# Kernel tuning notes

Hardware: AMD Instinct MI355X
Metric: run time of the kernel (lower is better)

Reference implementation:

```python
import jax, jax.numpy as jnp
import numpy as np

NB_LAYERS, KSIZE = 4, 5
DILATIONS = [1, 2, 4, 8]
NEG_SLOPE = 0.1
BN_EPS = 1e-5


def _cont_conv(times, feats, mask, dilation, p):
    """One ContConv1d layer: causal gather of time-diffs -> kernel MLP -> weighted aggregate + skip + BN."""
    k1W, k1b, k2W, k2b, k3W, k3b, skipW, skipb, gamma, beta = p
    bs, L, Cin = feats.shape
    Cout = skipW.shape[1]
    lags = jnp.arange(KSIZE) * dilation                    # (K,) include_zero_lag=True -> lag 0 included
    idx = jnp.arange(L)[None, :] - lags[:, None]           # (K, L) causal neighbor indices
    valid = idx >= 0
    idx_c = jnp.clip(idx, 0, L - 1)
    g_times = times[:, idx_c]                              # (bs, K, L)
    g_feats = feats[:, idx_c, :]                           # (bs, K, L, Cin)
    g_mask = (mask[:, idx_c] & valid[None] & mask[:, None, :]).astype(feats.dtype)
    dt = (times[:, None, :] - g_times) * g_mask            # (bs, K, L) zeroed where invalid
    # kernel MLP: scalar time-diff -> (Cin, Cout) mixing matrix
    h = jax.nn.leaky_relu(dt[..., None] @ k1W + k1b, NEG_SLOPE)
    h = jax.nn.leaky_relu(h @ k2W + k2b, NEG_SLOPE)
    kv = (h @ k3W + k3b).reshape(bs, KSIZE, L, Cin, Cout) * g_mask[..., None, None]
    out = jnp.einsum('bklc,bklcd->bld', g_feats, kv)       # aggregate over taps and input channels
    out = out + feats @ skipW + skipb                      # 1x1-conv skip connection
    mu = out.mean((0, 1))                                  # BatchNorm1d (training-mode batch stats)
    var = out.var((0, 1))
    return (out - mu) * jax.lax.rsqrt(var + BN_EPS) * gamma + beta


def _ccnn_forward(event_times, event_types, emb, k1W, k1b, k2W, k2b, k3W, k3b, skipW, skipb, gamma, beta):
    bs = event_times.shape[0]
    emb = emb.at[0].set(0.0)                               # padding_idx = 0
    times = jnp.concatenate([jnp.zeros((bs, 1), event_times.dtype), event_times], axis=1)
    bos = jnp.full((bs, 1), jnp.max(event_types) + 1, dtype=event_types.dtype)
    types = jnp.concatenate([bos, event_types], axis=1)
    mask = times != 0                                      # BOS (t=0) masked, as in the original
    enc = emb[types]                                       # (bs, L+1, C)
    for i in range(NB_LAYERS):
        p = (k1W[i], k1b[i], k2W[i], k2b[i], k3W[i], k3b[i], skipW[i], skipb[i], gamma[i], beta[i])
        enc = jax.nn.leaky_relu(_cont_conv(times, enc, mask, DILATIONS[i], p), NEG_SLOPE)
    return enc


def setup_inputs() -> dict:
    key = jax.random.key(0)
    ks = jax.random.split(key, 12)
    bs, L, C, H, num_types = 8, 2048, 32, 16, 100
    s = 0.05
    gaps = jax.random.uniform(ks[0], (bs, L)) * 0.1 + 0.01
    times = jnp.cumsum(gaps, axis=1)                       # strictly increasing positive event times
    types = jax.random.randint(ks[1], (bs, L), 0, num_types) + 1   # 1..num_types
    pad = jnp.arange(L) >= int(0.9 * L)
    times = jnp.where(pad[None, :], 0.0, times).astype(jnp.float32)
    types = jnp.where(pad[None, :], 0, types).astype(jnp.int32)
    return {
        'event_times': times,
        'event_types': types,
        'emb': jax.random.normal(ks[2], (num_types + 2, C)) * s,
        'k1W': jax.random.normal(ks[3], (NB_LAYERS, 1, H)) * s,
        'k1b': jnp.zeros((NB_LAYERS, H)),
        'k2W': jax.random.normal(ks[4], (NB_LAYERS, H, H)) * s,
        'k2b': jnp.zeros((NB_LAYERS, H)),
        'k3W': jax.random.normal(ks[5], (NB_LAYERS, H, C * C)) * s,
        'k3b': jnp.zeros((NB_LAYERS, C * C)),
        'skipW': jax.random.normal(ks[6], (NB_LAYERS, C, C)) * s,
        'skipb': jnp.zeros((NB_LAYERS, C)),
        'gamma': jnp.ones((NB_LAYERS, C)),
        'beta': jnp.zeros((NB_LAYERS, C)),
    }


def reference(event_times, event_types, emb, k1W, k1b, k2W, k2b, k3W, k3b, skipW, skipb, gamma, beta):
    return _ccnn_forward(event_times, event_types, emb, k1W, k1b, k2W, k2b, k3W, k3b, skipW, skipb, gamma, beta)
```

## Files before the change

kernel.cpp:

```cpp
#include <hip/hip_runtime.h>
#include <stdint.h>

#define NB_LAYERS 4
#define KSIZE 5
#define BSZ 8
#define LIN 2048
#define LSEQ 2049
#define CCH 32
#define HCH 16
#define MROWS (BSZ*LSEQ)
#define NTILES ((MROWS+15)/16)
#define NEG 0.1f
#define BNEPS 1e-5f
#define CONVGRID 129
#define CONVBLK 512
#define NFRAG 36
#define WT_HALVES (NFRAG*64*8)

typedef _Float16 h2v __attribute__((ext_vector_type(2)));
typedef _Float16 h8v __attribute__((ext_vector_type(8)));
typedef float    f4v __attribute__((ext_vector_type(4)));

union H8 { h8v v; h2v h[4]; };

static __device__ __forceinline__ h2v mkh2(float a, float b) {
  h2v r; r[0] = (_Float16)a; r[1] = (_Float16)b; return r;
}

static __device__ __forceinline__ void wt_decode(
    int g, const float* __restrict__ k3Wl, const float* __restrict__ k3bl,
    const float* __restrict__ skipWl, int& halfidx, float& val) {
  int n, k;
  if (g < 16384)      { n = g & 31; int c = (g >> 5) & 31; int h = g >> 10; k = h * 32 + c; val = k3Wl[g]; }
  else if (g < 17408) { int g2 = g - 16384; n = g2 & 31; int c = g2 >> 5; k = 512 + c; val = k3bl[g2]; }
  else                { int g2 = g - 17408; n = g2 & 31; int c = g2 >> 5; k = 544 + c; val = skipWl[g2]; }
  int m = n & 15, a = n >> 4, qq = (k >> 3) & 3, hh = k & 7;
  int f = (k < 512) ? ((k >> 5) * 2 + a) : ((k < 544) ? (32 + a) : (34 + a));
  halfidx = f * 512 + ((qq << 4) | m) * 8 + hh;
}

template<int MODE>
__global__ __launch_bounds__(CONVBLK) void conv_kernel(
    const float* __restrict__ enc_in,
    const int*   __restrict__ types,
    const float* __restrict__ emb,
    float* __restrict__ enc_out,
    const float* __restrict__ etimes,
    const float* __restrict__ k1Wp, const float* __restrict__ k1bp,
    const float* __restrict__ k2Wp, const float* __restrict__ k2bp,
    const float* __restrict__ k3W, const float* __restrict__ k3b,
    const float* __restrict__ skipW,
    _Float16* __restrict__ Wt,
    const float* __restrict__ stats_prev,
    const float* __restrict__ partials_prev,
    float* __restrict__ stats_out,
    float* __restrict__ partials_out,
    float* __restrict__ stats_zero,
    const float* __restrict__ gamma_prev, const float* __restrict__ beta_prev,
    int dil)
{
  __shared__ h8v swh[(CONVBLK/64) * KSIZE * 16 * 2];
  __shared__ alignas(16) float sW[304];
  __shared__ float sst[64];
  __shared__ float sbn[64];

  const int tid  = threadIdx.x;
  const int lane = tid & 63;
  const int wv   = tid >> 6;
  const int m    = lane & 15;
  const int q    = lane >> 4;

  if (tid < 64) { sst[tid] = 0.f; sbn[tid] = 0.f; }
  if (tid < 16) { sW[tid] = k1Wp[tid]; sW[16 + tid] = k1bp[tid]; sW[32 + tid] = k2bp[tid]; }
  if (tid >= 64 && tid < 320) sW[48 + tid - 64] = k2Wp[tid - 64];

  if (MODE == 0) {
    if (blockIdx.x == 0 && tid < 192) stats_zero[tid] = 0.f;
    int id2 = blockIdx.x * CONVBLK + tid;
    if (id2 < 3 * WT_HALVES) {
      int layer = 1 + id2 / WT_HALVES;
      int g = id2 - (layer - 1) * WT_HALVES;
      int hi; float val;
      wt_decode(g, k3W + layer * 16384, k3b + layer * 1024, skipW + layer * 1024, hi, val);
      Wt[(layer - 1) * WT_HALVES + hi] = (_Float16)val;
    }
  }
  __syncthreads();

  if (MODE == 1 && partials_prev) {
    float v = 0.f;
#pragma unroll 4
    for (int i = tid; i < CONVGRID * 64; i += CONVBLK) v += partials_prev[i];
    atomicAdd(&sbn[tid & 63], v);
    __syncthreads();
  }

  float sc8[8], ob8[8];
  if (MODE == 1) {
    const float inv = 1.f / (float)MROWS;
#pragma unroll
    for (int j = 0; j < 8; j++) {
      int c = q * 8 + j;
      float s1 = partials_prev ? sbn[c]      : stats_prev[c];
      float s2 = partials_prev ? sbn[32 + c] : stats_prev[32 + c];
      float mu = s1 * inv;
      float var = s2 * inv - mu * mu;
      float sc = gamma_prev[c] * rsqrtf(var + BNEPS);
      sc8[j] = sc; ob8[j] = beta_prev[c] - mu * sc;
    }
  }

  const int tile = blockIdx.x * (CONVBLK / 64) + wv;
  const bool deadtile = (tile >= NTILES);

  if (!deadtile) {
    int row = tile * 16 + m;
    bool rvalid = row < MROWS;
    int rowc = min(row, MROWS - 1);
    int b = rowc / LSEQ, pos = rowc % LSEQ;
    float t_l = (pos == 0) ? 0.f : etimes[b * LIN + pos - 1];
    bool mask_l = rvalid && (t_l != 0.f);

    int bosv = 0;
    if (MODE == 0) {
      if (__ballot(pos == 0)) {
        const int4* tp = (const int4*)types;
        int mx = 0;
#pragma unroll 4
        for (int i = lane; i < (BSZ * LIN) / 4; i += 64) {
          int4 v = tp[i];
          mx = max(mx, max(max(v.x, v.y), max(v.z, v.w)));
        }
#pragma unroll
        for (int off = 32; off; off >>= 1) mx = max(mx, __shfl_xor(mx, off, 64));
        bosv = mx + 1;
      }
    }

    int jcs[KSIZE]; float tjv[KSIZE];
#pragma unroll
    for (int tap = 0; tap < KSIZE; tap++) {
      int j = pos - tap * dil;
      int jc = max(j, 0); jcs[tap] = jc;
      tjv[tap] = (jc == 0) ? 0.f : etimes[b * LIN + jc - 1];
    }
    float4 fa[KSIZE], fbv[KSIZE];
    int tts[KSIZE];
    if (MODE == 0) {
#pragma unroll
      for (int tap = 0; tap < KSIZE; tap++) {
        int jc = jcs[tap];
        tts[tap] = (jc > 0) ? types[b * LIN + jc - 1] : ((tap == 0) ? bosv : 0);
      }
#pragma unroll
      for (int tap = 0; tap < KSIZE; tap++) {
        const float* ep = emb + tts[tap] * CCH + q * 8;
        fa[tap] = *(const float4*)ep; fbv[tap] = *(const float4*)(ep + 4);
      }
    } else {
#pragma unroll
      for (int tap = 0; tap < KSIZE; tap++) {
        const float* fp = enc_in + (b * LSEQ + jcs[tap]) * CCH + q * 8;
        fa[tap] = *(const float4*)fp; fbv[tap] = *(const float4*)(fp + 4);
      }
    }

    h2v fh[KSIZE][4];
    h2v fself[4];
    float Fb[8];
#pragma unroll
    for (int jj = 0; jj < 8; jj++) Fb[jj] = 0.f;

#pragma unroll
    for (int tap = 0; tap < KSIZE; tap++) {
      bool gm = mask_l && (pos - tap * dil >= 0) && (tjv[tap] != 0.f);
      float fv[8] = {fa[tap].x, fa[tap].y, fa[tap].z, fa[tap].w,
                     fbv[tap].x, fbv[tap].y, fbv[tap].z, fbv[tap].w};
      if (MODE == 0) {
        float zf = (tts[tap] != 0) ? 1.f : 0.f;
#pragma unroll
        for (int jj = 0; jj < 8; jj++) fv[jj] *= zf;
      } else {
#pragma unroll
        for (int jj = 0; jj < 8; jj++) {
          float x = fmaf(fv[jj], sc8[jj], ob8[jj]);
          fv[jj] = fmaxf(x, NEG * x);
        }
      }
      if (tap == 0) {
        float rv = rvalid ? 1.f : 0.f;
#pragma unroll
        for (int p2 = 0; p2 < 4; p2++) fself[p2] = mkh2(fv[2*p2] * rv, fv[2*p2+1] * rv);
      }
      float g = gm ? 1.f : 0.f;
#pragma unroll
      for (int jj = 0; jj < 8; jj++) Fb[jj] += g * fv[jj];
#pragma unroll
      for (int p2 = 0; p2 < 4; p2++) fh[tap][p2] = mkh2(fv[2*p2], fv[2*p2+1]);
    }

#pragma unroll
    for (int rep = 0; rep < 2; rep++) {
      const int jt = rep ? (KSIZE - 1) : (lane >> 4);
      const bool act = rep ? (lane < 16) : true;
      int j2 = pos - jt * dil;
      int jc2 = max(j2, 0);
      float tj2 = (jc2 == 0) ? 0.f : etimes[b * LIN + jc2 - 1];
      bool g2 = act && mask_l && (j2 >= 0) && (tj2 != 0.f);
      float dt = g2 ? (t_l - tj2) : 0.f;

      H8 w0, w1;
      if (__ballot(g2)) {
        const f4v* k1wv = (const f4v*)&sW[0];
        const f4v* k1bv = (const f4v*)&sW[16];
        const f4v* k2bv = (const f4v*)&sW[32];
        float h1[HCH], h2[HCH];
#pragma unroll
        for (int h4 = 0; h4 < 4; h4++) {
          f4v cw = k1wv[h4], cb = k1bv[h4], c2 = k2bv[h4];
#pragma unroll
          for (int r = 0; r < 4; r++) {
            float x = fmaf(dt, cw[r], cb[r]);
            h1[h4*4+r] = fmaxf(x, NEG * x);
            h2[h4*4+r] = c2[r];
          }
        }
#pragma unroll
        for (int hp = 0; hp < HCH; hp++) {
          float hv = h1[hp];
          const f4v* kk = (const f4v*)&sW[48 + hp * 16];
#pragma unroll
          for (int h4 = 0; h4 < 4; h4++) {
            f4v c = kk[h4];
#pragma unroll
            for (int r = 0; r < 4; r++) h2[h4*4+r] = fmaf(hv, c[r], h2[h4*4+r]);
          }
        }
        float g = g2 ? 1.f : 0.f;
#pragma unroll
        for (int p2 = 0; p2 < 4; p2++) {
          float a0 = h2[2*p2];     a0 = fmaxf(a0, NEG * a0) * g;
          float a1 = h2[2*p2+1];   a1 = fmaxf(a1, NEG * a1) * g;
          w0.h[p2] = mkh2(a0, a1);
          float b0 = h2[8+2*p2];   b0 = fmaxf(b0, NEG * b0) * g;
          float b1 = h2[8+2*p2+1]; b1 = fmaxf(b1, NEG * b1) * g;
          w1.h[p2] = mkh2(b0, b1);
        }
      } else {
#pragma unroll
        for (int p2 = 0; p2 < 4; p2++) { w0.h[p2] = mkh2(0.f, 0.f); w1.h[p2] = mkh2(0.f, 0.f); }
      }
      if (act) {
        int base = ((wv * KSIZE + jt) * 16 + m) * 2;
        swh[base] = w0.v; swh[base + 1] = w1.v;
      }
    }
    __syncthreads();

    h2v wh[KSIZE][8];
#pragma unroll
    for (int tap = 0; tap < KSIZE; tap++) {
      int base = ((wv * KSIZE + tap) * 16 + m) * 2;
      H8 a0, a1; a0.v = swh[base]; a1.v = swh[base + 1];
#pragma unroll
      for (int p2 = 0; p2 < 4; p2++) { wh[tap][p2] = a0.h[p2]; wh[tap][4+p2] = a1.h[p2]; }
    }

    f4v aP = {0,0,0,0}, aQ = {0,0,0,0}, bP = {0,0,0,0}, bQ = {0,0,0,0};

#pragma unroll
    for (int ks = 0; ks < 16; ks++) {
      H8 bf0, bf1, af;
      if (MODE == 0) {
        const float* wp = k3W + ks * 1024 + (q * 8) * 32 + m;
#pragma unroll
        for (int p2 = 0; p2 < 4; p2++) {
          bf0.h[p2] = mkh2(wp[(2*p2) * 32],      wp[(2*p2+1) * 32]);
          bf1.h[p2] = mkh2(wp[(2*p2) * 32 + 16], wp[(2*p2+1) * 32 + 16]);
        }
      } else {
        bf0.v = *(const h8v*)(Wt + (size_t)((2*ks + 0) * 64 + lane) * 8);
        bf1.v = *(const h8v*)(Wt + (size_t)((2*ks + 1) * 64 + lane) * 8);
      }
      h2v u0 = mkh2(0.f,0.f), u1 = mkh2(0.f,0.f), u2 = mkh2(0.f,0.f), u3 = mkh2(0.f,0.f);
#pragma unroll
      for (int tap = 0; tap < KSIZE; tap++) {
        _Float16 w = wh[tap][ks >> 1][ks & 1];
        h2v wd; wd[0] = w; wd[1] = w;
        u0 += wd * fh[tap][0];
        u1 += wd * fh[tap][1];
        u2 += wd * fh[tap][2];
        u3 += wd * fh[tap][3];
      }
      af.h[0] = u0; af.h[1] = u1; af.h[2] = u2; af.h[3] = u3;
      if (ks & 1) {
        aQ = __builtin_amdgcn_mfma_f32_16x16x32_f16(af.v, bf0.v, aQ, 0, 0, 0);
        bQ = __builtin_amdgcn_mfma_f32_16x16x32_f16(af.v, bf1.v, bQ, 0, 0, 0);
      } else {
        aP = __builtin_amdgcn_mfma_f32_16x16x32_f16(af.v, bf0.v, aP, 0, 0, 0);
        bP = __builtin_amdgcn_mfma_f32_16x16x32_f16(af.v, bf1.v, bP, 0, 0, 0);
      }
    }
    {
      H8 bf0, bf1, af;
      if (MODE == 0) {
        const float* kp = k3b + (q * 8) * 32 + m;
#pragma unroll
        for (int p2 = 0; p2 < 4; p2++) {
          bf0.h[p2] = mkh2(kp[(2*p2) * 32],      kp[(2*p2+1) * 32]);
          bf1.h[p2] = mkh2(kp[(2*p2) * 32 + 16], kp[(2*p2+1) * 32 + 16]);
        }
      } else {
        bf0.v = *(const h8v*)(Wt + (size_t)(32 * 64 + lane) * 8);
        bf1.v = *(const h8v*)(Wt + (size_t)(33 * 64 + lane) * 8);
      }
#pragma unroll
      for (int p2 = 0; p2 < 4; p2++) af.h[p2] = mkh2(Fb[2*p2], Fb[2*p2+1]);
      aP = __builtin_amdgcn_mfma_f32_16x16x32_f16(af.v, bf0.v, aP, 0, 0, 0);
      bP = __builtin_amdgcn_mfma_f32_16x16x32_f16(af.v, bf1.v, bP, 0, 0, 0);
    }
    {
      H8 bf0, bf1, af;
      if (MODE == 0) {
        const float* sp = skipW + (q * 8) * 32 + m;
#pragma unroll
        for (int p2 = 0; p2 < 4; p2++) {
          bf0.h[p2] = mkh2(sp[(2*p2) * 32],      sp[(2*p2+1) * 32]);
          bf1.h[p2] = mkh2(sp[(2*p2) * 32 + 16], sp[(2*p2+1) * 32 + 16]);
        }
      } else {
        bf0.v = *(const h8v*)(Wt + (size_t)(34 * 64 + lane) * 8);
        bf1.v = *(const h8v*)(Wt + (size_t)(35 * 64 + lane) * 8);
      }
      af.h[0] = fself[0]; af.h[1] = fself[1]; af.h[2] = fself[2]; af.h[3] = fself[3];
      aQ = __builtin_amdgcn_mfma_f32_16x16x32_f16(af.v, bf0.v, aQ, 0, 0, 0);
      bQ = __builtin_amdgcn_mfma_f32_16x16x32_f16(af.v, bf1.v, bQ, 0, 0, 0);
    }
    f4v acc0 = aP + aQ;
    f4v acc1 = bP + bQ;

    float s0 = 0.f, s1 = 0.f, s2 = 0.f, s3 = 0.f;
#pragma unroll
    for (int r = 0; r < 4; r++) {
      float v0 = acc0[r], v1 = acc1[r];
      s0 += v0; s1 += v0 * v0; s2 += v1; s3 += v1 * v1;
      int rd = tile * 16 + q * 4 + r;
      if (rd < MROWS) {
        enc_out[rd * CCH + m] = v0;
        enc_out[rd * CCH + 16 + m] = v1;
      }
    }
    s0 += __shfl_xor(s0, 16, 64); s0 += __shfl_xor(s0, 32, 64);
    s1 += __shfl_xor(s1, 16, 64); s1 += __shfl_xor(s1, 32, 64);
    s2 += __shfl_xor(s2, 16, 64); s2 += __shfl_xor(s2, 32, 64);
    s3 += __shfl_xor(s3, 16, 64); s3 += __shfl_xor(s3, 32, 64);
    if (q == 0) {
      atomicAdd(&sst[m], s0);
      atomicAdd(&sst[32 + m], s1);
      atomicAdd(&sst[16 + m], s2);
      atomicAdd(&sst[48 + m], s3);
    }
  } else {
    __syncthreads();
  }
  __syncthreads();
  if (tid < 64) {
    if (MODE == 0) partials_out[blockIdx.x * 64 + tid] = sst[tid];
    else           atomicAdd(&stats_out[tid], sst[tid]);
  }
}

__global__ __launch_bounds__(256) void bn_kernel(
    const float* __restrict__ x, float* __restrict__ out,
    const float* __restrict__ stats,
    const float* __restrict__ gamma, const float* __restrict__ beta) {
  int idx0 = blockIdx.x * 256 + threadIdx.x;
  int c0 = (idx0 * 4) & 31;
  const float inv = 1.f / (float)MROWS;
  float sc[4], ob[4];
#pragma unroll
  for (int r = 0; r < 4; r++) {
    int c = c0 + r;
    float mu = stats[c] * inv;
    float var = stats[32 + c] * inv - mu * mu;
    sc[r] = gamma[c] * rsqrtf(var + BNEPS);
    ob[r] = beta[c] - mu * sc[r];
  }
  for (int i = idx0; i < (MROWS * CCH) / 4; i += 256 * 256) {
    float4 v = ((const float4*)x)[i];
    float4 o;
    o.x = fmaf(v.x, sc[0], ob[0]); o.x = fmaxf(o.x, NEG * o.x);
    o.y = fmaf(v.y, sc[1], ob[1]); o.y = fmaxf(o.y, NEG * o.y);
    o.z = fmaf(v.z, sc[2], ob[2]); o.z = fmaxf(o.z, NEG * o.z);
    o.w = fmaf(v.w, sc[3], ob[3]); o.w = fmaxf(o.w, NEG * o.w);
    ((float4*)out)[i] = o;
  }
}

extern "C" void kernel_launch(void* const* d_in, const int* in_sizes, int n_in,
                              void* d_out, int out_size, void* d_ws, size_t ws_size,
                              hipStream_t stream) {
  (void)in_sizes; (void)n_in; (void)out_size; (void)ws_size;
  const float* event_times = (const float*)d_in[0];
  const int*   event_types = (const int*)d_in[1];
  const float* emb   = (const float*)d_in[2];
  const float* k1W   = (const float*)d_in[3];
  const float* k1b   = (const float*)d_in[4];
  const float* k2W   = (const float*)d_in[5];
  const float* k2b   = (const float*)d_in[6];
  const float* k3W   = (const float*)d_in[7];
  const float* k3b   = (const float*)d_in[8];
  const float* skipW = (const float*)d_in[9];
  const float* gamma = (const float*)d_in[11];
  const float* beta  = (const float*)d_in[12];

  float* enc_a = (float*)d_ws;
  float* enc_b = enc_a + (size_t)MROWS * CCH;
  float* stats = enc_b + (size_t)MROWS * CCH;
  float* partials0 = stats + NB_LAYERS * 64;
  _Float16* Wt = (_Float16*)(((uintptr_t)(partials0 + CONVGRID * 64) + 255) & ~(uintptr_t)255);

  conv_kernel<0><<<CONVGRID, CONVBLK, 0, stream>>>(
      nullptr, event_types, emb, enc_b, event_times,
      k1W, k1b, k2W, k2b, k3W, k3b, skipW, Wt,
      nullptr, nullptr, nullptr, partials0, stats + 64,
      nullptr, nullptr, 1);

  conv_kernel<1><<<CONVGRID, CONVBLK, 0, stream>>>(
      enc_b, nullptr, nullptr, enc_a, event_times,
      k1W + HCH, k1b + HCH, k2W + HCH*HCH, k2b + HCH,
      nullptr, nullptr, nullptr, Wt + 0 * WT_HALVES,
      nullptr, partials0, stats + 64, nullptr, nullptr,
      gamma + 0 * CCH, beta + 0 * CCH, 2);

  conv_kernel<1><<<CONVGRID, CONVBLK, 0, stream>>>(
      enc_a, nullptr, nullptr, enc_b, event_times,
      k1W + 2*HCH, k1b + 2*HCH, k2W + 2*HCH*HCH, k2b + 2*HCH,
      nullptr, nullptr, nullptr, Wt + 1 * WT_HALVES,
      stats + 64, nullptr, stats + 128, nullptr, nullptr,
      gamma + 1 * CCH, beta + 1 * CCH, 4);

  conv_kernel<1><<<CONVGRID, CONVBLK, 0, stream>>>(
      enc_b, nullptr, nullptr, enc_a, event_times,
      k1W + 3*HCH, k1b + 3*HCH, k2W + 3*HCH*HCH, k2b + 3*HCH,
      nullptr, nullptr, nullptr, Wt + 2 * WT_HALVES,
      stats + 128, nullptr, stats + 192, nullptr, nullptr,
      gamma + 2 * CCH, beta + 2 * CCH, 8);

  bn_kernel<<<256, 256, 0, stream>>>(enc_a, (float*)d_out,
      stats + 192, gamma + 3 * CCH, beta + 3 * CCH);
}
```

Before: 149.9 us.

## Stage fp16 weight fragments in LDS and rebalance kernel-MLP jobs across block

In MODE 1 the block now copies the pre-packed fp16 weight fragments (about 36 KB) from global memory into shared memory once, and the MFMA B-operands read from LDS instead of global. The per-tap kernel MLP work (5 taps x 16 rows per wave) is now spread across all threads of the block as 640 jobs, not done per wave with a mostly idle second pass, and the sync is restructured to match. The aim is to cut redundant global weight reads and improve lane utilization. The cost is a large LDS allocation that may reduce occupancy, plus extra index arithmetic and a second etimes gather per job.

```diff
diff --git a/kernel.cpp b/kernel.cpp
--- a/kernel.cpp
+++ b/kernel.cpp
@@ -14,6 +14,8 @@
 #define BNEPS 1e-5f
 #define CONVGRID 129
 #define CONVBLK 512
+#define NWAVES (CONVBLK/64)
+#define NJOBS (NWAVES*KSIZE*16)
 #define NFRAG 36
 #define WT_HALVES (NFRAG*64*8)
 
@@ -50,7 +52,7 @@
     const float* __restrict__ k2Wp, const float* __restrict__ k2bp,
     const float* __restrict__ k3W, const float* __restrict__ k3b,
     const float* __restrict__ skipW,
-    _Float16* __restrict__ Wt,
+    _Float16* __restrict__ WtG,
     const float* __restrict__ stats_prev,
     const float* __restrict__ partials_prev,
     float* __restrict__ stats_out,
@@ -59,7 +61,8 @@
     const float* __restrict__ gamma_prev, const float* __restrict__ beta_prev,
     int dil)
 {
-  __shared__ h8v swh[(CONVBLK/64) * KSIZE * 16 * 2];
+  __shared__ h8v Wl[(MODE == 1) ? (NFRAG * 64) : 1];
+  __shared__ h8v swh[NWAVES * KSIZE * 16 * 2];
   __shared__ alignas(16) float sW[304];
   __shared__ float sst[64];
   __shared__ float sbn[64];
@@ -69,20 +72,29 @@
   const int wv   = tid >> 6;
   const int m    = lane & 15;
   const int q    = lane >> 4;
+  const int bid  = blockIdx.x;
 
   if (tid < 64) { sst[tid] = 0.f; sbn[tid] = 0.f; }
   if (tid < 16) { sW[tid] = k1Wp[tid]; sW[16 + tid] = k1bp[tid]; sW[32 + tid] = k2bp[tid]; }
   if (tid >= 64 && tid < 320) sW[48 + tid - 64] = k2Wp[tid - 64];
 
   if (MODE == 0) {
-    if (blockIdx.x == 0 && tid < 192) stats_zero[tid] = 0.f;
-    int id2 = blockIdx.x * CONVBLK + tid;
+    if (bid == 0 && tid < 192) stats_zero[tid] = 0.f;
+    int id2 = bid * CONVBLK + tid;
     if (id2 < 3 * WT_HALVES) {
       int layer = 1 + id2 / WT_HALVES;
       int g = id2 - (layer - 1) * WT_HALVES;
       int hi; float val;
       wt_decode(g, k3W + layer * 16384, k3b + layer * 1024, skipW + layer * 1024, hi, val);
-      Wt[(layer - 1) * WT_HALVES + hi] = (_Float16)val;
+      WtG[(layer - 1) * WT_HALVES + hi] = (_Float16)val;
+    }
+  } else {
+    const float4* src = (const float4*)WtG;
+    float4* dst = (float4*)Wl;
+#pragma unroll
+    for (int i = 0; i < 5; i++) {
+      int idx = tid + i * CONVBLK;
+      if (idx < WT_HALVES / 8) dst[idx] = src[idx];
     }
   }
   __syncthreads();
@@ -110,17 +122,20 @@
     }
   }
 
-  const int tile = blockIdx.x * (CONVBLK / 64) + wv;
+  const int tile = bid * NWAVES + wv;
   const bool deadtile = (tile >= NTILES);
 
+  int row = tile * 16 + m;
+  bool rvalid = row < MROWS;
+  int rowc = min(row, MROWS - 1);
+  int b = rowc / LSEQ, pos = rowc % LSEQ;
+  float t_l = (pos == 0) ? 0.f : etimes[b * LIN + pos - 1];
+  bool mask_l = rvalid && (t_l != 0.f);
+
+  float4 fa[KSIZE], fbv[KSIZE];
+  int tts[KSIZE];
+  int jcs[KSIZE]; float tjv[KSIZE];
   if (!deadtile) {
-    int row = tile * 16 + m;
-    bool rvalid = row < MROWS;
-    int rowc = min(row, MROWS - 1);
-    int b = rowc / LSEQ, pos = rowc % LSEQ;
-    float t_l = (pos == 0) ? 0.f : etimes[b * LIN + pos - 1];
-    bool mask_l = rvalid && (t_l != 0.f);
-
     int bosv = 0;
     if (MODE == 0) {
       if (__ballot(pos == 0)) {
@@ -136,16 +151,12 @@
         bosv = mx + 1;
       }
     }
-
-    int jcs[KSIZE]; float tjv[KSIZE];
 #pragma unroll
     for (int tap = 0; tap < KSIZE; tap++) {
       int j = pos - tap * dil;
       int jc = max(j, 0); jcs[tap] = jc;
       tjv[tap] = (jc == 0) ? 0.f : etimes[b * LIN + jc - 1];
     }
-    float4 fa[KSIZE], fbv[KSIZE];
-    int tts[KSIZE];
     if (MODE == 0) {
 #pragma unroll
       for (int tap = 0; tap < KSIZE; tap++) {
@@ -164,13 +175,82 @@
         fa[tap] = *(const float4*)fp; fbv[tap] = *(const float4*)(fp + 4);
       }
     }
-
-    h2v fh[KSIZE][4];
-    h2v fself[4];
-    float Fb[8];
+  }
+
+#pragma unroll
+  for (int rep = 0; rep < 2; rep++) {
+    const int job = rep ? (512 + tid) : tid;
+    const bool act = rep ? (tid < 128) : true;
+    const int jj2 = act ? job : 0;
+    const int wvt = jj2 / 80;
+    const int rr  = jj2 % 80;
+    const int tap = rr / 16;
+    const int jrow = rr % 16;
+    const int tile_t = bid * NWAVES + wvt;
+    int row_t = tile_t * 16 + jrow;
+    bool rvalid_t = row_t < MROWS;
+    int rowc_t = min(row_t, MROWS - 1);
+    int b_t = rowc_t / LSEQ, pos_t = rowc_t % LSEQ;
+    float tl_t = (pos_t == 0) ? 0.f : etimes[b_t * LIN + pos_t - 1];
+    int j2 = pos_t - tap * dil;
+    int jc2 = max(j2, 0);
+    float tj2 = (jc2 == 0) ? 0.f : etimes[b_t * LIN + jc2 - 1];
+    bool g2 = act && rvalid_t && (tl_t != 0.f) && (j2 >= 0) && (tj2 != 0.f);
+    float dt = g2 ? (tl_t - tj2) : 0.f;
+
+    H8 w0, w1;
+    if (__ballot(g2)) {
+      const f4v* k1wv = (const f4v*)&sW[0];
+      const f4v* k1bv = (const f4v*)&sW[16];
+      const f4v* k2bv = (const f4v*)&sW[32];
+      float h1[HCH], h2[HCH];
+#pragma unroll
+      for (int h4 = 0; h4 < 4; h4++) {
+        f4v cw = k1wv[h4], cb = k1bv[h4], c2 = k2bv[h4];
+#pragma unroll
+        for (int r = 0; r < 4; r++) {
+          float x = fmaf(dt, cw[r], cb[r]);
+          h1[h4*4+r] = fmaxf(x, NEG * x);
+          h2[h4*4+r] = c2[r];
+        }
+      }
+#pragma unroll
+      for (int hp = 0; hp < HCH; hp++) {
+        float hv = h1[hp];
+        const f4v* kk = (const f4v*)&sW[48 + hp * 16];
+#pragma unroll
+        for (int h4 = 0; h4 < 4; h4++) {
+          f4v c = kk[h4];
+#pragma unroll
+          for (int r = 0; r < 4; r++) h2[h4*4+r] = fmaf(hv, c[r], h2[h4*4+r]);
+        }
+      }
+      float g = g2 ? 1.f : 0.f;
+#pragma unroll
+      for (int p2 = 0; p2 < 4; p2++) {
+        float a0 = h2[2*p2];     a0 = fmaxf(a0, NEG * a0) * g;
+        float a1 = h2[2*p2+1];   a1 = fmaxf(a1, NEG * a1) * g;
+        w0.h[p2] = mkh2(a0, a1);
+        float b0 = h2[8+2*p2];   b0 = fmaxf(b0, NEG * b0) * g;
+        float b1 = h2[8+2*p2+1]; b1 = fmaxf(b1, NEG * b1) * g;
+        w1.h[p2] = mkh2(b0, b1);
+      }
+    } else {
+#pragma unroll
+      for (int p2 = 0; p2 < 4; p2++) { w0.h[p2] = mkh2(0.f, 0.f); w1.h[p2] = mkh2(0.f, 0.f); }
+    }
+    if (act) {
+      int base = ((wvt * KSIZE + tap) * 16 + jrow) * 2;
+      swh[base] = w0.v; swh[base + 1] = w1.v;
+    }
+  }
+
+  h2v fh[KSIZE][4];
+  h2v fself[4];
+  float Fb[8];
+  if (!deadtile) {
 #pragma unroll
     for (int jj = 0; jj < 8; jj++) Fb[jj] = 0.f;
-
 #pragma unroll
     for (int tap = 0; tap < KSIZE; tap++) {
       bool gm = mask_l && (pos - tap * dil >= 0) && (tjv[tap] != 0.f);
@@ -198,65 +278,10 @@
 #pragma unroll
       for (int p2 = 0; p2 < 4; p2++) fh[tap][p2] = mkh2(fv[2*p2], fv[2*p2+1]);
     }
-
-#pragma unroll
-    for (int rep = 0; rep < 2; rep++) {
-      const int jt = rep ? (KSIZE - 1) : (lane >> 4);
-      const bool act = rep ? (lane < 16) : true;
-      int j2 = pos - jt * dil;
-      int jc2 = max(j2, 0);
-      float tj2 = (jc2 == 0) ? 0.f : etimes[b * LIN + jc2 - 1];
-      bool g2 = act && mask_l && (j2 >= 0) && (tj2 != 0.f);
-      float dt = g2 ? (t_l - tj2) : 0.f;
-
-      H8 w0, w1;
-      if (__ballot(g2)) {
-        const f4v* k1wv = (const f4v*)&sW[0];
-        const f4v* k1bv = (const f4v*)&sW[16];
-        const f4v* k2bv = (const f4v*)&sW[32];
-        float h1[HCH], h2[HCH];
-#pragma unroll
-        for (int h4 = 0; h4 < 4; h4++) {
-          f4v cw = k1wv[h4], cb = k1bv[h4], c2 = k2bv[h4];
-#pragma unroll
-          for (int r = 0; r < 4; r++) {
-            float x = fmaf(dt, cw[r], cb[r]);
-            h1[h4*4+r] = fmaxf(x, NEG * x);
-            h2[h4*4+r] = c2[r];
-          }
-        }
-#pragma unroll
-        for (int hp = 0; hp < HCH; hp++) {
-          float hv = h1[hp];
-          const f4v* kk = (const f4v*)&sW[48 + hp * 16];
-#pragma unroll
-          for (int h4 = 0; h4 < 4; h4++) {
-            f4v c = kk[h4];
-#pragma unroll
-            for (int r = 0; r < 4; r++) h2[h4*4+r] = fmaf(hv, c[r], h2[h4*4+r]);
-          }
-        }
-        float g = g2 ? 1.f : 0.f;
-#pragma unroll
-        for (int p2 = 0; p2 < 4; p2++) {
-          float a0 = h2[2*p2];     a0 = fmaxf(a0, NEG * a0) * g;
-          float a1 = h2[2*p2+1];   a1 = fmaxf(a1, NEG * a1) * g;
-          w0.h[p2] = mkh2(a0, a1);
-          float b0 = h2[8+2*p2];   b0 = fmaxf(b0, NEG * b0) * g;
-          float b1 = h2[8+2*p2+1]; b1 = fmaxf(b1, NEG * b1) * g;
-          w1.h[p2] = mkh2(b0, b1);
-        }
-      } else {
-#pragma unroll
-        for (int p2 = 0; p2 < 4; p2++) { w0.h[p2] = mkh2(0.f, 0.f); w1.h[p2] = mkh2(0.f, 0.f); }
-      }
-      if (act) {
-        int base = ((wv * KSIZE + jt) * 16 + m) * 2;
-        swh[base] = w0.v; swh[base + 1] = w1.v;
-      }
-    }
-    __syncthreads();
-
+  }
+  __syncthreads();
+
+  if (!deadtile) {
     h2v wh[KSIZE][8];
 #pragma unroll
     for (int tap = 0; tap < KSIZE; tap++) {
@@ -279,8 +304,8 @@
           bf1.h[p2] = mkh2(wp[(2*p2) * 32 + 16], wp[(2*p2+1) * 32 + 16]);
         }
       } else {
-        bf0.v = *(const h8v*)(Wt + (size_t)((2*ks + 0) * 64 + lane) * 8);
-        bf1.v = *(const h8v*)(Wt + (size_t)((2*ks + 1) * 64 + lane) * 8);
+        bf0.v = Wl[(2*ks + 0) * 64 + lane];
+        bf1.v = Wl[(2*ks + 1) * 64 + lane];
       }
       h2v u0 = mkh2(0.f,0.f), u1 = mkh2(0.f,0.f), u2 = mkh2(0.f,0.f), u3 = mkh2(0.f,0.f);
 #pragma unroll
@@ -311,8 +336,8 @@
           bf1.h[p2] = mkh2(kp[(2*p2) * 32 + 16], kp[(2*p2+1) * 32 + 16]);
         }
       } else {
-        bf0.v = *(const h8v*)(Wt + (size_t)(32 * 64 + lane) * 8);
-        bf1.v = *(const h8v*)(Wt + (size_t)(33 * 64 + lane) * 8);
+        bf0.v = Wl[32 * 64 + lane];
+        bf1.v = Wl[33 * 64 + lane];
       }
 #pragma unroll
       for (int p2 = 0; p2 < 4; p2++) af.h[p2] = mkh2(Fb[2*p2], Fb[2*p2+1]);
@@ -329,8 +354,8 @@
           bf1.h[p2] = mkh2(sp[(2*p2) * 32 + 16], sp[(2*p2+1) * 32 + 16]);
         }
       } else {
-        bf0.v = *(const h8v*)(Wt + (size_t)(34 * 64 + lane) * 8);
-        bf1.v = *(const h8v*)(Wt + (size_t)(35 * 64 + lane) * 8);
+        bf0.v = Wl[34 * 64 + lane];
+        bf1.v = Wl[35 * 64 + lane];
       }
       af.h[0] = fself[0]; af.h[1] = fself[1]; af.h[2] = fself[2]; af.h[3] = fself[3];
       aQ = __builtin_amdgcn_mfma_f32_16x16x32_f16(af.v, bf0.v, aQ, 0, 0, 0);
@@ -360,12 +385,10 @@
       atomicAdd(&sst[16 + m], s2);
       atomicAdd(&sst[48 + m], s3);
     }
-  } else {
-    __syncthreads();
   }
   __syncthreads();
   if (tid < 64) {
-    if (MODE == 0) partials_out[blockIdx.x * 64 + tid] = sst[tid];
+    if (MODE == 0) partials_out[bid * 64 + tid] = sst[tid];
     else           atomicAdd(&stats_out[tid], sst[tid]);
   }
 }
```

Result: faster. 143.9 us (median of 2 runs) (-4.0%).
